# Kernel optimization log

Measured on AMD Instinct MI355X. Metric: run time of the kernel, lower is better.

The kernel has to match this reference:

```python
import jax, jax.numpy as jnp
import numpy as np

N = 100000   # nodes
E = 500000   # edges per relation
D = 128      # in_dim == out_dim
R = 3        # relations
NEG_SLOPE = 0.2  # DGL GATConv default


def setup_inputs() -> dict:
    key = jax.random.key(0)
    ks = jax.random.split(key, 7)
    x = jax.random.normal(ks[0], (N, D), jnp.float32)
    src = jax.random.randint(ks[1], (R, E), 0, N, jnp.int32)
    dst = jax.random.randint(ks[2], (R, E), 0, N, jnp.int32)
    W = jax.random.normal(ks[3], (R, D, D), jnp.float32) * 0.05
    attn_l = jax.random.normal(ks[4], (R, D), jnp.float32) * 0.05
    attn_r = jax.random.normal(ks[5], (R, D), jnp.float32) * 0.05
    bias = jnp.zeros((R, D), jnp.float32)
    return {"x": x, "src": src, "dst": dst, "W": W,
            "attn_l": attn_l, "attn_r": attn_r, "bias": bias}


def _gat_rel(x, src, dst, W, al, ar, b):
    # GATConv, num_heads=1: project, per-edge attention, segment softmax over dst
    feat = x @ W.T                                   # [N, D]
    el = (feat * al).sum(-1)                         # [N]
    er = (feat * ar).sum(-1)                         # [N]
    e = jax.nn.leaky_relu(el[src] + er[dst], NEG_SLOPE)   # [E]
    m = jax.ops.segment_max(e, dst, num_segments=N)       # stable softmax max per dst
    ex = jnp.exp(e - m[dst])
    s = jax.ops.segment_sum(ex, dst, num_segments=N)
    alpha = ex / s[dst]                                    # edge softmax weights
    out = jax.ops.segment_sum(alpha[:, None] * feat[src], dst, num_segments=N)
    return out + b                                         # GATConv bias


def reference(x, src, dst, W, attn_l, attn_r, bias):
    # HeteroGraphConv(aggregate='mean') over relations, then squeeze(head dim)
    outs = [_gat_rel(x, src[r], dst[r], W[r], attn_l[r], attn_r[r], bias[r])
            for r in range(R)]
    return jnp.mean(jnp.stack(outs, axis=0), axis=0)
```

## Files before the change

### kernel.cpp

```cpp
#include <hip/hip_runtime.h>
#include <hip/hip_bf16.h>

#define NN 100000
#define DD 128
#define RR 3
#define EE 500000
#define CAP 44
#define BK 196
#define ECAP 8192
#define SELR 50176
#define GEMM_NB 782
#define PART_NB 733

using bf16 = __hip_bfloat16;
typedef __attribute__((ext_vector_type(8))) short short8;
typedef __attribute__((ext_vector_type(4))) float f32x4;

__device__ __forceinline__ unsigned short f2bf(float f) {
  unsigned int u = __float_as_uint(f);
  return (unsigned short)((u + 0x7fffu + ((u >> 16) & 1u)) >> 16);
}
__device__ __forceinline__ float blo(unsigned int u) { return __uint_as_float(u << 16); }
__device__ __forceinline__ float bhi(unsigned int u) { return __uint_as_float(u & 0xffff0000u); }

__device__ __forceinline__ void ld_lds16(const void* g, void* l) {
  __builtin_amdgcn_global_load_lds((const __attribute__((address_space(1))) unsigned int*)g,
                                   (__attribute__((address_space(3))) unsigned int*)l, 16, 0, 0);
}

__global__ __launch_bounds__(256) void k_pre(
    const float* __restrict__ W, const float* __restrict__ bias,
    short* __restrict__ Wb, float* __restrict__ bm, int* __restrict__ gcur)
{
  int idx = blockIdx.x * 256 + threadIdx.x;
  float4 v = ((const float4*)W)[idx];
  short4 s;
  s.x = (short)f2bf(v.x); s.y = (short)f2bf(v.y);
  s.z = (short)f2bf(v.z); s.w = (short)f2bf(v.w);
  ((short4*)Wb)[idx] = s;
  if (blockIdx.x == 0 && threadIdx.x < DD) {
    int t = threadIdx.x;
    bm[t] = (bias[t] + bias[DD + t] + bias[2 * DD + t]) * (1.f / 3.f);
  }
  if (blockIdx.x == 1 && threadIdx.x < BK) gcur[threadIdx.x] = 0;
}

__device__ __forceinline__ void gemm_body(
    char* smem, int bid,
    const float* __restrict__ x, const short* __restrict__ Wb,
    const float* __restrict__ attn_l, const float* __restrict__ attn_r,
    short* __restrict__ feat, float* __restrict__ el, float* __restrict__ er)
{
  const int t = threadIdx.x, lane = t & 63, wave = t >> 6;
  const int row0 = bid * 128;
  const int ml = lane & 15, q = lane >> 4;
  const int wr = wave >> 1, wc = wave & 1;

  {
    const int rbase = t >> 5, c4 = t & 31;
    const int chunk = c4 >> 1, half = c4 & 1;
    const int dst0 = ((chunk ^ (rbase & 7)) << 4) + (half << 3);
    const float4* x4 = (const float4*)x;
#pragma unroll 4
    for (int i = 0; i < 16; ++i) {
      int row = i * 8 + rbase;
      int grow = row0 + row; if (grow >= NN) grow = NN - 1;
      float4 v = x4[(size_t)grow * 32 + c4];
      unsigned int p0 = ((unsigned int)f2bf(v.y) << 16) | f2bf(v.x);
      unsigned int p1 = ((unsigned int)f2bf(v.w) << 16) | f2bf(v.z);
      *(uint2*)(smem + row * 256 + dst0) = make_uint2(p0, p1);
    }
  }

  int mbase[4], nbase[4];
#pragma unroll
  for (int i = 0; i < 4; ++i) {
    mbase[i] = (wr * 64 + i * 16 + ml) * 256;
    nbase[i] = 32768 + (wc * 64 + i * 16 + ml) * 256;
  }

  for (int rel = 0; rel < RR; ++rel) {
    if (rel) __syncthreads();
    {
      const int rloc = q & 3;
#pragma unroll
      for (int i = 0; i < 8; ++i) {
        int rowB = wave * 32 + i * 4 + rloc;
        int c = ml ^ (rowB & 7);
        const short* gp = Wb + (size_t)(rel * 128 + rowB) * 128 + c * 8;
        ld_lds16(gp, smem + 32768 + wave * 8192 + i * 1024);
      }
    }
    __syncthreads();

    f32x4 acc[4][4] = {};
#pragma unroll
    for (int kc = 0; kc < 4; ++kc) {
      const int sw = ((kc * 4 + q) ^ (ml & 7)) << 4;
      short8 av[4], bv[4];
#pragma unroll
      for (int i = 0; i < 4; ++i) av[i] = *(const short8*)(smem + mbase[i] + sw);
#pragma unroll
      for (int i = 0; i < 4; ++i) bv[i] = *(const short8*)(smem + nbase[i] + sw);
#pragma unroll
      for (int mi = 0; mi < 4; ++mi)
#pragma unroll
        for (int ni = 0; ni < 4; ++ni)
          acc[mi][ni] = __builtin_amdgcn_mfma_f32_16x16x32_bf16(av[mi], bv[ni], acc[mi][ni], 0, 0, 0);
    }

    float pel[4][4], per_[4][4];
    {
      float alv[4], arv[4];
#pragma unroll
      for (int ni = 0; ni < 4; ++ni) {
        int c = rel * DD + wc * 64 + ni * 16 + ml;
        alv[ni] = attn_l[c]; arv[ni] = attn_r[c];
      }
#pragma unroll
      for (int mi = 0; mi < 4; ++mi)
#pragma unroll
        for (int reg = 0; reg < 4; ++reg) {
          float se = 0.f, sr = 0.f;
#pragma unroll
          for (int ni = 0; ni < 4; ++ni) {
            se = fmaf(acc[mi][ni][reg], alv[ni], se);
            sr = fmaf(acc[mi][ni][reg], arv[ni], sr);
          }
          pel[mi][reg] = se; per_[mi][reg] = sr;
        }
#pragma unroll
      for (int msk = 1; msk < 16; msk <<= 1)
#pragma unroll
        for (int mi = 0; mi < 4; ++mi)
#pragma unroll
          for (int reg = 0; reg < 4; ++reg) {
            pel[mi][reg]  += __shfl_xor(pel[mi][reg], msk);
            per_[mi][reg] += __shfl_xor(per_[mi][reg], msk);
          }
    }

    char* fb = (char*)feat + (size_t)rel * NN * 256;
#pragma unroll
    for (int p = 0; p < 2; ++p) {
      __syncthreads();
      if (p == 0 && ml == 0) {
#pragma unroll
        for (int mi = 0; mi < 4; ++mi)
#pragma unroll
          for (int reg = 0; reg < 4; ++reg) {
            int row = wr * 64 + mi * 16 + q * 4 + reg;
            *(float*)(smem + SELR + row * 16 + wc * 4)     = pel[mi][reg];
            *(float*)(smem + SELR + row * 16 + 8 + wc * 4) = per_[mi][reg];
          }
      }
      if (wr == p) {
#pragma unroll
        for (int mi = 0; mi < 4; ++mi)
#pragma unroll
          for (int ni = 0; ni < 4; ++ni) {
            f32x4 v = acc[mi][ni];
#pragma unroll
            for (int reg = 0; reg < 4; ++reg) {
              int rl = mi * 16 + q * 4 + reg;
              *(short*)(smem + 32768 + rl * 272 + wc * 128 + ni * 32 + ml * 2) = (short)f2bf(v[reg]);
            }
          }
      }
      __syncthreads();
      if (p == 0 && t < 128 && row0 + t < NN) {
        float4 v = *(const float4*)(smem + SELR + t * 16);
        el[rel * NN + row0 + t] = v.x + v.y;
        er[rel * NN + row0 + t] = v.z + v.w;
      }
#pragma unroll
      for (int o = 0; o < 4; ++o) {
        int rl = o * 16 + (t >> 4);
        int coloff = (t & 15) * 16;
        int grow = row0 + p * 64 + rl;
        if (grow < NN) {
          int4 v = *(const int4*)(smem + 32768 + rl * 272 + coloff);
          *(int4*)(fb + (size_t)grow * 256 + coloff) = v;
        }
      }
    }
  }
}

__device__ __forceinline__ void part_body(
    char* smem, int vb,
    const int* __restrict__ src, const int* __restrict__ dst,
    int* __restrict__ gcur, int* __restrict__ ebuf)
{
  int* lh = (int*)smem;
  const int t = threadIdx.x;
  for (int b = t; b < BK; b += 256) lh[b] = 0;
  __syncthreads();

  int eb[8], ebk[8];
  const int base = vb * 2048 + t;
#pragma unroll
  for (int k = 0; k < 8; ++k) {
    int i = base + k * 256;
    ebk[k] = -1;
    if (i < RR * EE) {
      int d = __builtin_nontemporal_load(&dst[i]);
      int s = __builtin_nontemporal_load(&src[i]);
      int r = i >= 2 * EE ? 2 : (i >= EE ? 1 : 0);
      ebk[k] = d >> 9;
      eb[k] = ((d & 511) << 19) | (r << 17) | s;
      atomicAdd(&lh[ebk[k]], 1);
    }
  }
  __syncthreads();
  if (t < BK) {
    int v = lh[t];
    lh[t] = v ? atomicAdd(&gcur[t], v) : 0;
  }
  __syncthreads();
#pragma unroll
  for (int k = 0; k < 8; ++k) {
    if (ebk[k] >= 0) {
      int pos = atomicAdd(&lh[ebk[k]], 1);
      if (pos < ECAP) ebuf[ebk[k] * ECAP + pos] = eb[k];
    }
  }
}

__global__ __launch_bounds__(256, 2) void k_fused(
    const float* __restrict__ x, const short* __restrict__ Wb,
    const float* __restrict__ attn_l, const float* __restrict__ attn_r,
    short* __restrict__ feat, float* __restrict__ el, float* __restrict__ er,
    const int* __restrict__ src, const int* __restrict__ dst,
    int* __restrict__ gcur, int* __restrict__ ebuf)
{
  __shared__ __align__(16) char smem[65536];
  if (blockIdx.x < GEMM_NB) {
    gemm_body(smem, blockIdx.x, x, Wb, attn_l, attn_r, feat, el, er);
  } else {
    part_body(smem, blockIdx.x - GEMM_NB, src, dst, gcur, ebuf);
  }
}

__global__ __launch_bounds__(256) void k_build(
    const int* __restrict__ gcur, const int* __restrict__ ebuf,
    int* __restrict__ counts, int* __restrict__ payload)
{
  __shared__ int lcnt[512];
  const int b = blockIdx.x, t = threadIdx.x;
  lcnt[t] = 0; lcnt[t + 256] = 0;
  __syncthreads();
  int cnt = gcur[b]; if (cnt > ECAP) cnt = ECAP;
  const int n0 = b << 9;
  for (int i = t; i < cnt; i += 256) {
    int ent = ebuf[b * ECAP + i];
    int dlow = ent >> 19;
    int pos = atomicAdd(&lcnt[dlow], 1);
    if (pos < CAP)
      payload[(size_t)(n0 + dlow) * CAP + pos] = ((ent >> 17) & 3) * NN + (ent & 0x1FFFF);
  }
  __syncthreads();
  if (n0 + t < NN)       counts[n0 + t] = lcnt[t];
  if (n0 + t + 256 < NN) counts[n0 + t + 256] = lcnt[t + 256];
}

__global__ __launch_bounds__(256) void k_gather(
    const int* __restrict__ counts, const int* __restrict__ payload,
    const float* __restrict__ el, const float* __restrict__ er,
    const short* __restrict__ feat, const float* __restrict__ bm,
    float* __restrict__ out)
{
  const int lane = threadIdx.x & 63;
  const int hw = lane >> 4, m = lane & 15;
  const int n = blockIdx.x * 4 + (threadIdx.x >> 6);
  int deg = counts[n];
  deg = deg > CAP ? CAP : deg;
  const float er0 = er[n], er1 = er[NN + n], er2 = er[2 * NN + n];
  const bool act = lane < deg;
  int pl = act ? payload[(size_t)n * CAP + lane] : 0;
  int r = pl >= 2 * NN ? 2 : (pl >= NN ? 1 : 0);
  float ex = 0.f;
  if (act) {
    float e = el[pl] + (r == 0 ? er0 : (r == 1 ? er1 : er2));
    e = e >= 0.f ? e : 0.2f * e;
    ex = __expf(e);
  }
  float v0 = (act && r == 0) ? ex : 0.f;
  float v1 = (act && r == 1) ? ex : 0.f;
  float v2 = (act && r == 2) ? ex : 0.f;
#pragma unroll
  for (int msk = 1; msk < 64; msk <<= 1) {
    v0 += __shfl_xor(v0, msk);
    v1 += __shfl_xor(v1, msk);
    v2 += __shfl_xor(v2, msk);
  }
  float i0 = v0 > 0.f ? 1.f / v0 : 0.f;
  float i1 = v1 > 0.f ? 1.f / v1 : 0.f;
  float i2 = v2 > 0.f ? 1.f / v2 : 0.f;
  float w = ex * (r == 0 ? i0 : (r == 1 ? i1 : i2));

  float a8[8] = {0.f, 0.f, 0.f, 0.f, 0.f, 0.f, 0.f, 0.f};
  const unsigned short* fs = (const unsigned short*)feat;

#define FETCH16(E, W0, W1, W2, W3, U0, U1, U2, U3)                        \
  do {                                                                    \
    int i0_ = (E) + hw, i1_ = (E) + 4 + hw, i2_ = (E) + 8 + hw,           \
        i3_ = (E) + 12 + hw;                                              \
    W0 = __shfl(w, i0_); W1 = __shfl(w, i1_);                             \
    W2 = __shfl(w, i2_); W3 = __shfl(w, i3_);                             \
    int p0_ = __shfl(pl, i0_), p1_ = __shfl(pl, i1_),                     \
        p2_ = __shfl(pl, i2_), p3_ = __shfl(pl, i3_);                     \
    U0 = *(const uint4*)(fs + (size_t)p0_ * DD + m * 8);                  \
    U1 = *(const uint4*)(fs + (size_t)p1_ * DD + m * 8);                  \
    U2 = *(const uint4*)(fs + (size_t)p2_ * DD + m * 8);                  \
    U3 = *(const uint4*)(fs + (size_t)p3_ * DD + m * 8);                  \
  } while (0)

#define FMA8(WE, U)                                                       \
  do {                                                                    \
    a8[0] = fmaf(WE, blo(U.x), a8[0]); a8[1] = fmaf(WE, bhi(U.x), a8[1]); \
    a8[2] = fmaf(WE, blo(U.y), a8[2]); a8[3] = fmaf(WE, bhi(U.y), a8[3]); \
    a8[4] = fmaf(WE, blo(U.z), a8[4]); a8[5] = fmaf(WE, bhi(U.z), a8[5]); \
    a8[6] = fmaf(WE, blo(U.w), a8[6]); a8[7] = fmaf(WE, bhi(U.w), a8[7]); \
  } while (0)

  if (deg > 0) {
    float cw0, cw1, cw2, cw3;
    uint4 cu0, cu1, cu2, cu3;
    FETCH16(0, cw0, cw1, cw2, cw3, cu0, cu1, cu2, cu3);
    for (int e = 16; e < deg; e += 16) {
      float nw0, nw1, nw2, nw3;
      uint4 nu0, nu1, nu2, nu3;
      FETCH16(e, nw0, nw1, nw2, nw3, nu0, nu1, nu2, nu3);
      FMA8(cw0, cu0); FMA8(cw1, cu1); FMA8(cw2, cu2); FMA8(cw3, cu3);
      cw0 = nw0; cw1 = nw1; cw2 = nw2; cw3 = nw3;
      cu0 = nu0; cu1 = nu1; cu2 = nu2; cu3 = nu3;
    }
    FMA8(cw0, cu0); FMA8(cw1, cu1); FMA8(cw2, cu2); FMA8(cw3, cu3);
  }
#undef FETCH16
#undef FMA8

#pragma unroll
  for (int k = 0; k < 8; ++k) {
    a8[k] += __shfl_xor(a8[k], 16);
    a8[k] += __shfl_xor(a8[k], 32);
  }
  if (hw == 0) {
    const int j = m * 8;
    float4 b0 = *(const float4*)(bm + j);
    float4 b1 = *(const float4*)(bm + j + 4);
    float4 o0, o1;
    o0.x = a8[0] * (1.f / 3.f) + b0.x; o0.y = a8[1] * (1.f / 3.f) + b0.y;
    o0.z = a8[2] * (1.f / 3.f) + b0.z; o0.w = a8[3] * (1.f / 3.f) + b0.w;
    o1.x = a8[4] * (1.f / 3.f) + b1.x; o1.y = a8[5] * (1.f / 3.f) + b1.y;
    o1.z = a8[6] * (1.f / 3.f) + b1.z; o1.w = a8[7] * (1.f / 3.f) + b1.w;
    float* op = out + (size_t)n * DD + j;
    *(float4*)op = o0;
    *(float4*)(op + 4) = o1;
  }
}

extern "C" void kernel_launch(void* const* d_in, const int* in_sizes, int n_in,
                              void* d_out, int out_size, void* d_ws, size_t ws_size,
                              hipStream_t stream)
{
  const float* x    = (const float*)d_in[0];
  const int*   src  = (const int*)d_in[1];
  const int*   dst  = (const int*)d_in[2];
  const float* W    = (const float*)d_in[3];
  const float* al   = (const float*)d_in[4];
  const float* ar   = (const float*)d_in[5];
  const float* bias = (const float*)d_in[6];
  float* out = (float*)d_out;

  char* p = (char*)d_ws;
  short* feat    = (short*)p; p += (size_t)RR * NN * DD * 2;
  int*   payload = (int*)p;   p += (size_t)NN * CAP * 4;
  int*   ebuf    = (int*)p;   p += (size_t)BK * ECAP * 4;
  float* el      = (float*)p; p += (size_t)RR * NN * 4;
  float* er      = (float*)p; p += (size_t)RR * NN * 4;
  short* Wb      = (short*)p; p += (size_t)RR * DD * DD * 2;
  float* bm      = (float*)p; p += (size_t)DD * 4;
  int*   counts  = (int*)p;   p += (size_t)NN * 4;
  int*   gcur    = (int*)p;   p += (size_t)BK * 4;

  k_pre<<<48, 256, 0, stream>>>(W, bias, Wb, bm, gcur);
  k_fused<<<GEMM_NB + PART_NB, 256, 0, stream>>>(x, Wb, al, ar, feat, el, er,
                                                 src, dst, gcur, ebuf);
  k_build<<<BK, 256, 0, stream>>>(gcur, ebuf, counts, payload);
  k_gather<<<NN / 4, 256, 0, stream>>>(counts, payload, el, er, feat, bm, out);
}
```

Baseline: 245.1 us.

## Widen fused GEMM blocks to 512 threads with register-held A fragments

The fused GEMM/partition kernel now launches 512 threads per block. Each of eight waves computes a 32x64 tile instead of 64x64, so the accumulator footprint per thread is halved. The x rows are loaded straight from global memory into register bf16 MFMA fragments, which drops the LDS staging of x. W is staged with ordinary vector loads instead of global_load_lds, and the epilogue writes all 128 rows in one pass with fewer barriers. In exchange, partition blocks leave half their threads idle, LDS use per block grows, and the 512,4 launch bound may force a tight register budget and cause spills.

```diff
diff --git a/kernel.cpp b/kernel.cpp
--- a/kernel.cpp
+++ b/kernel.cpp
@@ -8,9 +8,11 @@
 #define CAP 44
 #define BK 196
 #define ECAP 8192
-#define SELR 50176
 #define GEMM_NB 782
 #define PART_NB 733
+#define EPIOFF 32768
+#define SELR2 67584
+#define SMEMSZ 69632
 
 using bf16 = __hip_bfloat16;
 typedef __attribute__((ext_vector_type(8))) short short8;
@@ -22,11 +24,6 @@
 }
 __device__ __forceinline__ float blo(unsigned int u) { return __uint_as_float(u << 16); }
 __device__ __forceinline__ float bhi(unsigned int u) { return __uint_as_float(u & 0xffff0000u); }
-
-__device__ __forceinline__ void ld_lds16(const void* g, void* l) {
-  __builtin_amdgcn_global_load_lds((const __attribute__((address_space(1))) unsigned int*)g,
-                                   (__attribute__((address_space(3))) unsigned int*)l, 16, 0, 0);
-}
 
 __global__ __launch_bounds__(256) void k_pre(
     const float* __restrict__ W, const float* __restrict__ bias,
@@ -56,60 +53,55 @@
   const int ml = lane & 15, q = lane >> 4;
   const int wr = wave >> 1, wc = wave & 1;
 
-  {
-    const int rbase = t >> 5, c4 = t & 31;
-    const int chunk = c4 >> 1, half = c4 & 1;
-    const int dst0 = ((chunk ^ (rbase & 7)) << 4) + (half << 3);
-    const float4* x4 = (const float4*)x;
-#pragma unroll 4
-    for (int i = 0; i < 16; ++i) {
-      int row = i * 8 + rbase;
-      int grow = row0 + row; if (grow >= NN) grow = NN - 1;
-      float4 v = x4[(size_t)grow * 32 + c4];
-      unsigned int p0 = ((unsigned int)f2bf(v.y) << 16) | f2bf(v.x);
-      unsigned int p1 = ((unsigned int)f2bf(v.w) << 16) | f2bf(v.z);
-      *(uint2*)(smem + row * 256 + dst0) = make_uint2(p0, p1);
-    }
-  }
-
-  int mbase[4], nbase[4];
-#pragma unroll
-  for (int i = 0; i < 4; ++i) {
-    mbase[i] = (wr * 64 + i * 16 + ml) * 256;
-    nbase[i] = 32768 + (wc * 64 + i * 16 + ml) * 256;
-  }
+  short8 av[2][4];
+#pragma unroll
+  for (int mi = 0; mi < 2; ++mi) {
+    int grow = row0 + wr * 32 + mi * 16 + ml; if (grow >= NN) grow = NN - 1;
+    const float* xr = x + (size_t)grow * DD;
+#pragma unroll
+    for (int kc = 0; kc < 4; ++kc) {
+      float4 v0 = *(const float4*)(xr + kc * 32 + q * 8);
+      float4 v1 = *(const float4*)(xr + kc * 32 + q * 8 + 4);
+      short8 a;
+      a[0] = (short)f2bf(v0.x); a[1] = (short)f2bf(v0.y);
+      a[2] = (short)f2bf(v0.z); a[3] = (short)f2bf(v0.w);
+      a[4] = (short)f2bf(v1.x); a[5] = (short)f2bf(v1.y);
+      a[6] = (short)f2bf(v1.z); a[7] = (short)f2bf(v1.w);
+      av[mi][kc] = a;
+    }
+  }
+
+  int nbase[4];
+#pragma unroll
+  for (int i = 0; i < 4; ++i) nbase[i] = (wc * 64 + i * 16 + ml) * 256;
 
   for (int rel = 0; rel < RR; ++rel) {
-    if (rel) __syncthreads();
-    {
-      const int rloc = q & 3;
-#pragma unroll
-      for (int i = 0; i < 8; ++i) {
-        int rowB = wave * 32 + i * 4 + rloc;
-        int c = ml ^ (rowB & 7);
-        const short* gp = Wb + (size_t)(rel * 128 + rowB) * 128 + c * 8;
-        ld_lds16(gp, smem + 32768 + wave * 8192 + i * 1024);
-      }
-    }
     __syncthreads();
 
-    f32x4 acc[4][4] = {};
+#pragma unroll
+    for (int rnd = 0; rnd < 4; ++rnd) {
+      int r = (t >> 4) + rnd * 32;
+      int c = t & 15;
+      uint4 w4 = *(const uint4*)(Wb + (size_t)(rel * 128 + r) * 128 + c * 8);
+      *(uint4*)(smem + r * 256 + ((c ^ (r & 7)) << 4)) = w4;
+    }
+    __syncthreads();
+
+    f32x4 acc[2][4] = {};
 #pragma unroll
     for (int kc = 0; kc < 4; ++kc) {
       const int sw = ((kc * 4 + q) ^ (ml & 7)) << 4;
-      short8 av[4], bv[4];
-#pragma unroll
-      for (int i = 0; i < 4; ++i) av[i] = *(const short8*)(smem + mbase[i] + sw);
+      short8 bv[4];
 #pragma unroll
       for (int i = 0; i < 4; ++i) bv[i] = *(const short8*)(smem + nbase[i] + sw);
 #pragma unroll
-      for (int mi = 0; mi < 4; ++mi)
+      for (int mi = 0; mi < 2; ++mi)
 #pragma unroll
         for (int ni = 0; ni < 4; ++ni)
-          acc[mi][ni] = __builtin_amdgcn_mfma_f32_16x16x32_bf16(av[mi], bv[ni], acc[mi][ni], 0, 0, 0);
-    }
-
-    float pel[4][4], per_[4][4];
+          acc[mi][ni] = __builtin_amdgcn_mfma_f32_16x16x32_bf16(av[mi][kc], bv[ni], acc[mi][ni], 0, 0, 0);
+    }
+
+    float pel[2][4], per_[2][4];
     {
       float alv[4], arv[4];
 #pragma unroll
@@ -118,7 +110,7 @@
         alv[ni] = attn_l[c]; arv[ni] = attn_r[c];
       }
 #pragma unroll
-      for (int mi = 0; mi < 4; ++mi)
+      for (int mi = 0; mi < 2; ++mi)
 #pragma unroll
         for (int reg = 0; reg < 4; ++reg) {
           float se = 0.f, sr = 0.f;
@@ -132,7 +124,7 @@
 #pragma unroll
       for (int msk = 1; msk < 16; msk <<= 1)
 #pragma unroll
-        for (int mi = 0; mi < 4; ++mi)
+        for (int mi = 0; mi < 2; ++mi)
 #pragma unroll
           for (int reg = 0; reg < 4; ++reg) {
             pel[mi][reg]  += __shfl_xor(pel[mi][reg], msk);
@@ -140,48 +132,43 @@
           }
     }
 
+#pragma unroll
+    for (int mi = 0; mi < 2; ++mi)
+#pragma unroll
+      for (int ni = 0; ni < 4; ++ni) {
+        f32x4 v = acc[mi][ni];
+#pragma unroll
+        for (int reg = 0; reg < 4; ++reg) {
+          int rl = wr * 32 + mi * 16 + q * 4 + reg;
+          *(short*)(smem + EPIOFF + rl * 272 + wc * 128 + ni * 32 + ml * 2) = (short)f2bf(v[reg]);
+        }
+      }
+    if (ml == 0) {
+#pragma unroll
+      for (int mi = 0; mi < 2; ++mi)
+#pragma unroll
+        for (int reg = 0; reg < 4; ++reg) {
+          int row = wr * 32 + mi * 16 + q * 4 + reg;
+          *(float*)(smem + SELR2 + row * 16 + wc * 4)     = pel[mi][reg];
+          *(float*)(smem + SELR2 + row * 16 + 8 + wc * 4) = per_[mi][reg];
+        }
+    }
+    __syncthreads();
+
     char* fb = (char*)feat + (size_t)rel * NN * 256;
-#pragma unroll
-    for (int p = 0; p < 2; ++p) {
-      __syncthreads();
-      if (p == 0 && ml == 0) {
-#pragma unroll
-        for (int mi = 0; mi < 4; ++mi)
-#pragma unroll
-          for (int reg = 0; reg < 4; ++reg) {
-            int row = wr * 64 + mi * 16 + q * 4 + reg;
-            *(float*)(smem + SELR + row * 16 + wc * 4)     = pel[mi][reg];
-            *(float*)(smem + SELR + row * 16 + 8 + wc * 4) = per_[mi][reg];
-          }
-      }
-      if (wr == p) {
-#pragma unroll
-        for (int mi = 0; mi < 4; ++mi)
-#pragma unroll
-          for (int ni = 0; ni < 4; ++ni) {
-            f32x4 v = acc[mi][ni];
-#pragma unroll
-            for (int reg = 0; reg < 4; ++reg) {
-              int rl = mi * 16 + q * 4 + reg;
-              *(short*)(smem + 32768 + rl * 272 + wc * 128 + ni * 32 + ml * 2) = (short)f2bf(v[reg]);
-            }
-          }
-      }
-      __syncthreads();
-      if (p == 0 && t < 128 && row0 + t < NN) {
-        float4 v = *(const float4*)(smem + SELR + t * 16);
-        el[rel * NN + row0 + t] = v.x + v.y;
-        er[rel * NN + row0 + t] = v.z + v.w;
-      }
-#pragma unroll
-      for (int o = 0; o < 4; ++o) {
-        int rl = o * 16 + (t >> 4);
-        int coloff = (t & 15) * 16;
-        int grow = row0 + p * 64 + rl;
-        if (grow < NN) {
-          int4 v = *(const int4*)(smem + 32768 + rl * 272 + coloff);
-          *(int4*)(fb + (size_t)grow * 256 + coloff) = v;
-        }
+    if (t < 128 && row0 + t < NN) {
+      float4 v = *(const float4*)(smem + SELR2 + t * 16);
+      el[rel * NN + row0 + t] = v.x + v.y;
+      er[rel * NN + row0 + t] = v.z + v.w;
+    }
+#pragma unroll
+    for (int o = 0; o < 4; ++o) {
+      int rl = o * 32 + (t >> 4);
+      int coloff = (t & 15) * 16;
+      int grow = row0 + rl;
+      if (grow < NN) {
+        int4 v = *(const int4*)(smem + EPIOFF + rl * 272 + coloff);
+        *(int4*)(fb + (size_t)grow * 256 + coloff) = v;
       }
     }
   }
@@ -194,22 +181,25 @@
 {
   int* lh = (int*)smem;
   const int t = threadIdx.x;
-  for (int b = t; b < BK; b += 256) lh[b] = 0;
+  if (t < BK) lh[t] = 0;
   __syncthreads();
 
   int eb[8], ebk[8];
-  const int base = vb * 2048 + t;
-#pragma unroll
-  for (int k = 0; k < 8; ++k) {
-    int i = base + k * 256;
-    ebk[k] = -1;
-    if (i < RR * EE) {
-      int d = __builtin_nontemporal_load(&dst[i]);
-      int s = __builtin_nontemporal_load(&src[i]);
-      int r = i >= 2 * EE ? 2 : (i >= EE ? 1 : 0);
-      ebk[k] = d >> 9;
-      eb[k] = ((d & 511) << 19) | (r << 17) | s;
-      atomicAdd(&lh[ebk[k]], 1);
+#pragma unroll
+  for (int k = 0; k < 8; ++k) ebk[k] = -1;
+  if (t < 256) {
+    const int base = vb * 2048 + t;
+#pragma unroll
+    for (int k = 0; k < 8; ++k) {
+      int i = base + k * 256;
+      if (i < RR * EE) {
+        int d = __builtin_nontemporal_load(&dst[i]);
+        int s = __builtin_nontemporal_load(&src[i]);
+        int r = i >= 2 * EE ? 2 : (i >= EE ? 1 : 0);
+        ebk[k] = d >> 9;
+        eb[k] = ((d & 511) << 19) | (r << 17) | s;
+        atomicAdd(&lh[ebk[k]], 1);
+      }
     }
   }
   __syncthreads();
@@ -227,14 +217,14 @@
   }
 }
 
-__global__ __launch_bounds__(256, 2) void k_fused(
+__global__ __launch_bounds__(512, 4) void k_fused(
     const float* __restrict__ x, const short* __restrict__ Wb,
     const float* __restrict__ attn_l, const float* __restrict__ attn_r,
     short* __restrict__ feat, float* __restrict__ el, float* __restrict__ er,
     const int* __restrict__ src, const int* __restrict__ dst,
     int* __restrict__ gcur, int* __restrict__ ebuf)
 {
-  __shared__ __align__(16) char smem[65536];
+  __shared__ __align__(16) char smem[SMEMSZ];
   if (blockIdx.x < GEMM_NB) {
     gemm_body(smem, blockIdx.x, x, Wb, attn_l, attn_r, feat, el, er);
   } else {
@@ -386,7 +376,7 @@
   int*   gcur    = (int*)p;   p += (size_t)BK * 4;
 
   k_pre<<<48, 256, 0, stream>>>(W, bias, Wb, bm, gcur);
-  k_fused<<<GEMM_NB + PART_NB, 256, 0, stream>>>(x, Wb, al, ar, feat, el, er,
+  k_fused<<<GEMM_NB + PART_NB, 512, 0, stream>>>(x, Wb, al, ar, feat, el, er,
                                                  src, dst, gcur, ebuf);
   k_build<<<BK, 256, 0, stream>>>(gcur, ebuf, counts, payload);
   k_gather<<<NN / 4, 256, 0, stream>>>(counts, payload, el, er, feat, bm, out);
```

Result: slower. 261.5 us (+6.7%).

## Fuse bucket build into fused kernel via completion counter; use packed FMA in gather

Applied to the files above, without the earlier changes.

Moves the k_build stage into k_fused as extra trailing blocks. Each one spins on a global atomic counter that partition blocks increment once their ebuf writes are fenced, which removes one kernel launch and the boundary between launches. The gather inner loop is also rewritten to use two-wide float vector FMAs on bf16-unpacked pairs, so the compiler can emit packed FMA instructions. The spin-wait relies on all partition blocks being scheduled before, or alongside, the waiting build blocks. Waiting blocks also hold CU slots that GEMM or partition blocks could otherwise use.

```diff
diff --git a/kernel.cpp b/kernel.cpp
--- a/kernel.cpp
+++ b/kernel.cpp
@@ -15,13 +15,18 @@
 using bf16 = __hip_bfloat16;
 typedef __attribute__((ext_vector_type(8))) short short8;
 typedef __attribute__((ext_vector_type(4))) float f32x4;
+typedef __attribute__((ext_vector_type(2))) float f32x2;
 
 __device__ __forceinline__ unsigned short f2bf(float f) {
   unsigned int u = __float_as_uint(f);
   return (unsigned short)((u + 0x7fffu + ((u >> 16) & 1u)) >> 16);
 }
-__device__ __forceinline__ float blo(unsigned int u) { return __uint_as_float(u << 16); }
-__device__ __forceinline__ float bhi(unsigned int u) { return __uint_as_float(u & 0xffff0000u); }
+__device__ __forceinline__ f32x2 bf2f2(unsigned int u) {
+  f32x2 r;
+  r[0] = __uint_as_float(u << 16);
+  r[1] = __uint_as_float(u & 0xffff0000u);
+  return r;
+}
 
 __device__ __forceinline__ void ld_lds16(const void* g, void* l) {
   __builtin_amdgcn_global_load_lds((const __attribute__((address_space(1))) unsigned int*)g,
@@ -42,7 +47,7 @@
     int t = threadIdx.x;
     bm[t] = (bias[t] + bias[DD + t] + bias[2 * DD + t]) * (1.f / 3.f);
   }
-  if (blockIdx.x == 1 && threadIdx.x < BK) gcur[threadIdx.x] = 0;
+  if (blockIdx.x == 1 && threadIdx.x <= BK) gcur[threadIdx.x] = 0;
 }
 
 __device__ __forceinline__ void gemm_body(
@@ -227,27 +232,13 @@
   }
 }
 
-__global__ __launch_bounds__(256, 2) void k_fused(
-    const float* __restrict__ x, const short* __restrict__ Wb,
-    const float* __restrict__ attn_l, const float* __restrict__ attn_r,
-    short* __restrict__ feat, float* __restrict__ el, float* __restrict__ er,
-    const int* __restrict__ src, const int* __restrict__ dst,
-    int* __restrict__ gcur, int* __restrict__ ebuf)
-{
-  __shared__ __align__(16) char smem[65536];
-  if (blockIdx.x < GEMM_NB) {
-    gemm_body(smem, blockIdx.x, x, Wb, attn_l, attn_r, feat, el, er);
-  } else {
-    part_body(smem, blockIdx.x - GEMM_NB, src, dst, gcur, ebuf);
-  }
-}
-
-__global__ __launch_bounds__(256) void k_build(
+__device__ __forceinline__ void build_body(
+    char* smem, int b,
     const int* __restrict__ gcur, const int* __restrict__ ebuf,
     int* __restrict__ counts, int* __restrict__ payload)
 {
-  __shared__ int lcnt[512];
-  const int b = blockIdx.x, t = threadIdx.x;
+  int* lcnt = (int*)smem;
+  const int t = threadIdx.x;
   lcnt[t] = 0; lcnt[t + 256] = 0;
   __syncthreads();
   int cnt = gcur[b]; if (cnt > ECAP) cnt = ECAP;
@@ -262,6 +253,36 @@
   __syncthreads();
   if (n0 + t < NN)       counts[n0 + t] = lcnt[t];
   if (n0 + t + 256 < NN) counts[n0 + t + 256] = lcnt[t + 256];
+}
+
+__global__ __launch_bounds__(256, 2) void k_fused(
+    const float* __restrict__ x, const short* __restrict__ Wb,
+    const float* __restrict__ attn_l, const float* __restrict__ attn_r,
+    short* __restrict__ feat, float* __restrict__ el, float* __restrict__ er,
+    const int* __restrict__ src, const int* __restrict__ dst,
+    int* __restrict__ gcur, int* __restrict__ ebuf,
+    int* __restrict__ counts, int* __restrict__ payload)
+{
+  __shared__ __align__(16) char smem[65536];
+  const unsigned b = blockIdx.x;
+  if (b < GEMM_NB) {
+    gemm_body(smem, b, x, Wb, attn_l, attn_r, feat, el, er);
+  } else if (b < GEMM_NB + PART_NB) {
+    part_body(smem, b - GEMM_NB, src, dst, gcur, ebuf);
+    __syncthreads();
+    if (threadIdx.x == 0) {
+      __threadfence();
+      atomicAdd(&gcur[BK], 1);
+    }
+  } else {
+    if (threadIdx.x == 0) {
+      while (__hip_atomic_load(&gcur[BK], __ATOMIC_ACQUIRE, __HIP_MEMORY_SCOPE_AGENT) < PART_NB)
+        __builtin_amdgcn_s_sleep(8);
+      __threadfence();
+    }
+    __syncthreads();
+    build_body(smem, b - GEMM_NB - PART_NB, gcur, ebuf, counts, payload);
+  }
 }
 
 __global__ __launch_bounds__(256) void k_gather(
@@ -299,7 +320,7 @@
   float i2 = v2 > 0.f ? 1.f / v2 : 0.f;
   float w = ex * (r == 0 ? i0 : (r == 1 ? i1 : i2));
 
-  float a8[8] = {0.f, 0.f, 0.f, 0.f, 0.f, 0.f, 0.f, 0.f};
+  f32x2 a2[4] = {};
   const unsigned short* fs = (const unsigned short*)feat;
 
 #define FETCH16(E, W0, W1, W2, W3, U0, U1, U2, U3)                        \
@@ -318,10 +339,11 @@
 
 #define FMA8(WE, U)                                                       \
   do {                                                                    \
-    a8[0] = fmaf(WE, blo(U.x), a8[0]); a8[1] = fmaf(WE, bhi(U.x), a8[1]); \
-    a8[2] = fmaf(WE, blo(U.y), a8[2]); a8[3] = fmaf(WE, bhi(U.y), a8[3]); \
-    a8[4] = fmaf(WE, blo(U.z), a8[4]); a8[5] = fmaf(WE, bhi(U.z), a8[5]); \
-    a8[6] = fmaf(WE, blo(U.w), a8[6]); a8[7] = fmaf(WE, bhi(U.w), a8[7]); \
+    f32x2 w2_; w2_[0] = WE; w2_[1] = WE;                                  \
+    a2[0] = __builtin_elementwise_fma(w2_, bf2f2(U.x), a2[0]);            \
+    a2[1] = __builtin_elementwise_fma(w2_, bf2f2(U.y), a2[1]);            \
+    a2[2] = __builtin_elementwise_fma(w2_, bf2f2(U.z), a2[2]);            \
+    a2[3] = __builtin_elementwise_fma(w2_, bf2f2(U.w), a2[3]);            \
   } while (0)
 
   if (deg > 0) {
@@ -341,6 +363,9 @@
 #undef FETCH16
 #undef FMA8
 
+  float a8[8];
+#pragma unroll
+  for (int k = 0; k < 8; ++k) a8[k] = a2[k >> 1][k & 1];
 #pragma unroll
   for (int k = 0; k < 8; ++k) {
     a8[k] += __shfl_xor(a8[k], 16);
@@ -383,11 +408,10 @@
   short* Wb      = (short*)p; p += (size_t)RR * DD * DD * 2;
   float* bm      = (float*)p; p += (size_t)DD * 4;
   int*   counts  = (int*)p;   p += (size_t)NN * 4;
-  int*   gcur    = (int*)p;   p += (size_t)BK * 4;
+  int*   gcur    = (int*)p;   p += (size_t)(BK + 1) * 4;
 
   k_pre<<<48, 256, 0, stream>>>(W, bias, Wb, bm, gcur);
-  k_fused<<<GEMM_NB + PART_NB, 256, 0, stream>>>(x, Wb, al, ar, feat, el, er,
-                                                 src, dst, gcur, ebuf);
-  k_build<<<BK, 256, 0, stream>>>(gcur, ebuf, counts, payload);
+  k_fused<<<GEMM_NB + PART_NB + BK, 256, 0, stream>>>(
+      x, Wb, al, ar, feat, el, er, src, dst, gcur, ebuf, counts, payload);
   k_gather<<<NN / 4, 256, 0, stream>>>(counts, payload, el, er, feat, bm, out);
 }
```

Result: slower. 330.7 us (+34.9%).
